# Kernel optimization log

Hardware: AMD Instinct MI355X
Metric: run time of the kernel (lower is better)

The kernel has to match this reference:

```python
import jax, jax.numpy as jnp
import numpy as np

B, D, STRIDE, OUT = 8192, 1024, 16, 64
L = D // STRIDE


def setup_inputs() -> dict:
    key = jax.random.key(0)
    kx, kw, kb = jax.random.split(key, 3)
    x = jax.random.normal(kx, (B, D), dtype=jnp.float32)
    # Stacked per-layer Dense kernels: layer i only sees features j < i*STRIDE.
    # Glorot-ish scale; masked entries are zeroed in reference() (faithful: they
    # don't exist in the original per-layer kernels).
    W = jax.random.normal(kw, (L, D, OUT), dtype=jnp.float32) * 0.02
    b = jax.random.normal(kb, (L, OUT), dtype=jnp.float32) * 0.02
    return {"x": x, "W": W, "b": b}


def reference(x, W, b):
    # Original: tf.stack([Dense_i(x[..., :i*stride]) for i in range(L)], -2)
    # Equivalent single causal-masked batched matmul.
    Lx, Dx, Ox = W.shape
    stride = Dx // Lx
    # mask[l, d] = 1 if feature d is visible to layer l (d < l*stride)
    mask = (jnp.arange(Dx)[None, :] < (jnp.arange(Lx) * stride)[:, None]).astype(W.dtype)
    Wm = W * mask[:, :, None]                      # [L, D, O]
    out = jnp.einsum("bd,ldo->blo", x, Wm) + b    # [B, L, O]
    return out
```

## Files before the change

kernel.cpp:

```cpp
#include <hip/hip_runtime.h>
#include <hip/hip_bf16.h>
#include <stdint.h>

#define BROWS 8192
#define DDIM  1024
#define LDIM  64
#define ODIM  64
#define NDIM  4096
#define KSTRIDE 16

typedef __attribute__((ext_vector_type(8))) short bf16x8;
typedef __attribute__((ext_vector_type(4))) float f32x4;
typedef __attribute__((ext_vector_type(8))) unsigned short u16x8;

static __device__ __forceinline__ unsigned short f2bf(float f) {
    union { float f; uint32_t u; } v; v.f = f;
    uint32_t r = 0x7FFFu + ((v.u >> 16) & 1u);
    return (unsigned short)((v.u + r) >> 16);
}

static __device__ __forceinline__ void async16(const void* g, void* l) {
    __builtin_amdgcn_global_load_lds(
        (const __attribute__((address_space(1))) void*)g,
        (__attribute__((address_space(3))) void*)l, 16, 0, 0);
}

__global__ __launch_bounds__(256) void cvt_x_kernel(const float* __restrict__ x,
                                                    unsigned short* __restrict__ xb) {
    int i = blockIdx.x * 256 + threadIdx.x;
    const float4* xf = reinterpret_cast<const float4*>(x);
    float4 v0 = xf[2 * i];
    float4 v1 = xf[2 * i + 1];
    u16x8 r;
    r[0] = f2bf(v0.x); r[1] = f2bf(v0.y); r[2] = f2bf(v0.z); r[3] = f2bf(v0.w);
    r[4] = f2bf(v1.x); r[5] = f2bf(v1.y); r[6] = f2bf(v1.z); r[7] = f2bf(v1.w);
    reinterpret_cast<u16x8*>(xb)[i] = r;
}

__global__ __launch_bounds__(256) void prep_w_kernel(const float* __restrict__ W,
                                                     unsigned short* __restrict__ wbt) {
    __shared__ float tile[64][65];
    const int l  = blockIdx.x >> 4;
    const int d0 = (blockIdx.x & 15) << 6;
    const int t  = threadIdx.x;
    {
        const int dd = t >> 2;
        const int o4 = (t & 3) << 4;
        const float* src = W + ((size_t)((l << 10) + d0 + dd) << 6) + o4;
        #pragma unroll
        for (int j = 0; j < 4; ++j) {
            float4 v = reinterpret_cast<const float4*>(src)[j];
            tile[dd][o4 + 4 * j + 0] = v.x;
            tile[dd][o4 + 4 * j + 1] = v.y;
            tile[dd][o4 + 4 * j + 2] = v.z;
            tile[dd][o4 + 4 * j + 3] = v.w;
        }
    }
    __syncthreads();
    {
        const int o    = t >> 2;
        const int dloc = (t & 3) << 4;
        const int kmax = l * KSTRIDE;
        unsigned short* dst = wbt + ((size_t)((l << 6) + o) << 10) + d0 + dloc;
        u16x8 r0, r1;
        #pragma unroll
        for (int j = 0; j < 8; ++j) {
            int da = d0 + dloc + j;
            int db = da + 8;
            r0[j] = (da < kmax) ? f2bf(tile[dloc + j][o])     : (unsigned short)0;
            r1[j] = (db < kmax) ? f2bf(tile[dloc + 8 + j][o]) : (unsigned short)0;
        }
        *reinterpret_cast<u16x8*>(dst)     = r0;
        *reinterpret_cast<u16x8*>(dst + 8) = r1;
    }
}

__global__ __launch_bounds__(256, 2) void ar_gemm_kernel(
        const unsigned short* __restrict__ xb,
        const unsigned short* __restrict__ wbt,
        const float* __restrict__ bias,
        float* __restrict__ out) {
    __shared__ unsigned short As[128 * 32];
    __shared__ unsigned short Bs[128 * 32];

    const int bm   = blockIdx.x & 63;
    const int bn   = 31 - (blockIdx.x >> 6);
    const int tid  = threadIdx.x;
    const int lane = tid & 63;
    const int wave = tid >> 6;
    const int wr   = wave >> 1;
    const int wc   = wave & 1;

    const int nkt = ((2 * bn + 1) * KSTRIDE + 31) >> 5;

    const int rc = lane >> 2;
    const int cb = (lane & 3) << 4;
    const char* gA0 = (const char*)xb  + ((size_t)(bm * 128 + (2 * wave + 0) * 16 + rc) * 2048) + cb;
    const char* gA1 = (const char*)xb  + ((size_t)(bm * 128 + (2 * wave + 1) * 16 + rc) * 2048) + cb;
    const char* gB0 = (const char*)wbt + ((size_t)(bn * 128 + (2 * wave + 0) * 16 + rc) * 2048) + cb;
    const char* gB1 = (const char*)wbt + ((size_t)(bn * 128 + (2 * wave + 1) * 16 + rc) * 2048) + cb;
    char* lA0 = (char*)As + (2 * wave + 0) * 1024;
    char* lA1 = (char*)As + (2 * wave + 1) * 1024;
    char* lB0 = (char*)Bs + (2 * wave + 0) * 1024;
    char* lB1 = (char*)Bs + (2 * wave + 1) * 1024;

    const int aoff = ((wr << 6) + (lane & 15)) * 64 + ((lane >> 4) << 4);
    const int boff = ((wc << 6) + (lane & 15)) * 64 + ((lane >> 4) << 4);

    f32x4 acc[4][4];
    #pragma unroll
    for (int m = 0; m < 4; ++m)
        #pragma unroll
        for (int n = 0; n < 4; ++n)
            acc[m][n] = (f32x4)(0.f);

    for (int kt = 0; kt < nkt; ++kt) {
        const int kb = kt << 6;
        async16(gA0 + kb, lA0);
        async16(gA1 + kb, lA1);
        async16(gB0 + kb, lB0);
        async16(gB1 + kb, lB1);
        __syncthreads();
        bf16x8 a[4], b[4];
        #pragma unroll
        for (int m = 0; m < 4; ++m)
            a[m] = *reinterpret_cast<const bf16x8*>((const char*)As + aoff + m * 1024);
        #pragma unroll
        for (int n = 0; n < 4; ++n)
            b[n] = *reinterpret_cast<const bf16x8*>((const char*)Bs + boff + n * 1024);
        #pragma unroll
        for (int m = 0; m < 4; ++m)
            #pragma unroll
            for (int n = 0; n < 4; ++n)
                acc[m][n] = __builtin_amdgcn_mfma_f32_16x16x32_bf16(a[m], b[n], acc[m][n], 0, 0, 0);
        __syncthreads();
    }

    const int crow = (bm << 7) + (wr << 6) + ((lane >> 4) << 2);
    const int ccol = (bn << 7) + (wc << 6) + (lane & 15);
    float bv[4];
    #pragma unroll
    for (int n = 0; n < 4; ++n) bv[n] = bias[ccol + n * 16];
    #pragma unroll
    for (int m = 0; m < 4; ++m)
        #pragma unroll
        for (int n = 0; n < 4; ++n)
            #pragma unroll
            for (int j = 0; j < 4; ++j)
                out[(size_t)(crow + m * 16 + j) * NDIM + ccol + n * 16] = acc[m][n][j] + bv[n];
}

__global__ __launch_bounds__(256) void naive_kernel(const float* __restrict__ x,
                                                    const float* __restrict__ W,
                                                    const float* __restrict__ bias,
                                                    float* __restrict__ out) {
    size_t idx = (size_t)blockIdx.x * 256 + threadIdx.x;
    if (idx >= (size_t)BROWS * NDIM) return;
    int m = (int)(idx >> 12);
    int n = (int)(idx & 4095);
    int l = n >> 6;
    int o = n & 63;
    int kmax = l * KSTRIDE;
    float s = bias[n];
    const float* xr = x + (size_t)m * DDIM;
    const float* wp = W + ((size_t)l << 16) + o;
    for (int d = 0; d < kmax; ++d) s += xr[d] * wp[(size_t)d << 6];
    out[idx] = s;
}

extern "C" void kernel_launch(void* const* d_in, const int* in_sizes, int n_in,
                              void* d_out, int out_size, void* d_ws, size_t ws_size,
                              hipStream_t stream) {
    const float* x = (const float*)d_in[0];
    const float* W = (const float*)d_in[1];
    const float* b = (const float*)d_in[2];
    float* out = (float*)d_out;

    const size_t need = ((size_t)BROWS * DDIM + (size_t)NDIM * DDIM) * sizeof(unsigned short);
    if (ws_size < need) {
        int total = BROWS * NDIM;
        naive_kernel<<<(total + 255) / 256, 256, 0, stream>>>(x, W, b, out);
        return;
    }
    unsigned short* xbuf = (unsigned short*)d_ws;
    unsigned short* wbt  = xbuf + (size_t)BROWS * DDIM;

    cvt_x_kernel<<<(BROWS * DDIM) / (256 * 8), 256, 0, stream>>>(x, xbuf);
    prep_w_kernel<<<LDIM * 16, 256, 0, stream>>>(W, wbt);
    ar_gemm_kernel<<<64 * 32, 256, 0, stream>>>(xbuf, wbt, b, out);
}
```

Baseline: 66.70 us.

## Rewrite GEMM as 256x256 double-buffered pipelined kernel and fuse prep kernels

```diff
diff --git a/kernel.cpp b/kernel.cpp
--- a/kernel.cpp
+++ b/kernel.cpp
@@ -25,129 +25,199 @@
         (__attribute__((address_space(3))) void*)l, 16, 0, 0);
 }
 
-__global__ __launch_bounds__(256) void cvt_x_kernel(const float* __restrict__ x,
-                                                    unsigned short* __restrict__ xb) {
-    int i = blockIdx.x * 256 + threadIdx.x;
-    const float4* xf = reinterpret_cast<const float4*>(x);
-    float4 v0 = xf[2 * i];
-    float4 v1 = xf[2 * i + 1];
-    u16x8 r;
-    r[0] = f2bf(v0.x); r[1] = f2bf(v0.y); r[2] = f2bf(v0.z); r[3] = f2bf(v0.w);
-    r[4] = f2bf(v1.x); r[5] = f2bf(v1.y); r[6] = f2bf(v1.z); r[7] = f2bf(v1.w);
-    reinterpret_cast<u16x8*>(xb)[i] = r;
-}
-
-__global__ __launch_bounds__(256) void prep_w_kernel(const float* __restrict__ W,
-                                                     unsigned short* __restrict__ wbt) {
-    __shared__ float tile[64][65];
-    const int l  = blockIdx.x >> 4;
-    const int d0 = (blockIdx.x & 15) << 6;
-    const int t  = threadIdx.x;
-    {
-        const int dd = t >> 2;
-        const int o4 = (t & 3) << 4;
-        const float* src = W + ((size_t)((l << 10) + d0 + dd) << 6) + o4;
-        #pragma unroll
-        for (int j = 0; j < 4; ++j) {
-            float4 v = reinterpret_cast<const float4*>(src)[j];
-            tile[dd][o4 + 4 * j + 0] = v.x;
-            tile[dd][o4 + 4 * j + 1] = v.y;
-            tile[dd][o4 + 4 * j + 2] = v.z;
-            tile[dd][o4 + 4 * j + 3] = v.w;
-        }
+__global__ __launch_bounds__(256) void prep_kernel(const float* __restrict__ x,
+                                                   const float* __restrict__ W,
+                                                   unsigned short* __restrict__ xb,
+                                                   unsigned short* __restrict__ wbt) {
+    const int bid = blockIdx.x;
+    if (bid < 1024) {
+        __shared__ float tile[64][65];
+        const int l  = bid >> 4;
+        const int d0 = (bid & 15) << 6;
+        const int t  = threadIdx.x;
+        {
+            const int dd = t >> 2;
+            const int o4 = (t & 3) << 4;
+            const float* src = W + ((size_t)((l << 10) + d0 + dd) << 6) + o4;
+            #pragma unroll
+            for (int j = 0; j < 4; ++j) {
+                float4 v = reinterpret_cast<const float4*>(src)[j];
+                tile[dd][o4 + 4 * j + 0] = v.x;
+                tile[dd][o4 + 4 * j + 1] = v.y;
+                tile[dd][o4 + 4 * j + 2] = v.z;
+                tile[dd][o4 + 4 * j + 3] = v.w;
+            }
+        }
+        __syncthreads();
+        {
+            const int o    = t >> 2;
+            const int dloc = (t & 3) << 4;
+            const int kmax = l * KSTRIDE;
+            unsigned short* dst = wbt + ((size_t)((l << 6) + o) << 10) + d0 + dloc;
+            u16x8 r0, r1;
+            #pragma unroll
+            for (int j = 0; j < 8; ++j) {
+                int da = d0 + dloc + j;
+                int db = da + 8;
+                r0[j] = (da < kmax) ? f2bf(tile[dloc + j][o])     : (unsigned short)0;
+                r1[j] = (db < kmax) ? f2bf(tile[dloc + 8 + j][o]) : (unsigned short)0;
+            }
+            *reinterpret_cast<u16x8*>(dst)     = r0;
+            *reinterpret_cast<u16x8*>(dst + 8) = r1;
+        }
+    } else {
+        int i = (bid - 1024) * 256 + threadIdx.x;
+        const float4* xf = reinterpret_cast<const float4*>(x);
+        float4 v0 = xf[2 * i];
+        float4 v1 = xf[2 * i + 1];
+        u16x8 r;
+        r[0] = f2bf(v0.x); r[1] = f2bf(v0.y); r[2] = f2bf(v0.z); r[3] = f2bf(v0.w);
+        r[4] = f2bf(v1.x); r[5] = f2bf(v1.y); r[6] = f2bf(v1.z); r[7] = f2bf(v1.w);
+        reinterpret_cast<u16x8*>(xb)[i] = r;
     }
-    __syncthreads();
-    {
-        const int o    = t >> 2;
-        const int dloc = (t & 3) << 4;
-        const int kmax = l * KSTRIDE;
-        unsigned short* dst = wbt + ((size_t)((l << 6) + o) << 10) + d0 + dloc;
-        u16x8 r0, r1;
-        #pragma unroll
-        for (int j = 0; j < 8; ++j) {
-            int da = d0 + dloc + j;
-            int db = da + 8;
-            r0[j] = (da < kmax) ? f2bf(tile[dloc + j][o])     : (unsigned short)0;
-            r1[j] = (db < kmax) ? f2bf(tile[dloc + 8 + j][o]) : (unsigned short)0;
-        }
-        *reinterpret_cast<u16x8*>(dst)     = r0;
-        *reinterpret_cast<u16x8*>(dst + 8) = r1;
-    }
-}
-
-__global__ __launch_bounds__(256, 2) void ar_gemm_kernel(
+}
+
+#define MMQ(I0, J0, B) \
+    _Pragma("unroll") \
+    for (int ii = 0; ii < 4; ++ii) \
+    _Pragma("unroll") \
+    for (int jj = 0; jj < 2; ++jj) \
+    _Pragma("unroll") \
+    for (int kk = 0; kk < 2; ++kk) \
+        acc[(I0) + ii][(J0) + jj] = __builtin_amdgcn_mfma_f32_16x16x32_bf16( \
+            a[ii][kk], B[jj][kk], acc[(I0) + ii][(J0) + jj], 0, 0, 0);
+
+#define BAR_MID() do { __builtin_amdgcn_s_barrier(); \
+    asm volatile("s_waitcnt lgkmcnt(0)" ::: "memory"); \
+    __builtin_amdgcn_sched_barrier(0); } while (0)
+#define BAR_END() do { __builtin_amdgcn_sched_barrier(0); \
+    __builtin_amdgcn_s_barrier(); } while (0)
+#define VMW4() asm volatile("s_waitcnt vmcnt(4)" ::: "memory")
+
+__global__ __launch_bounds__(512, 2) void ar_gemm_kernel(
         const unsigned short* __restrict__ xb,
         const unsigned short* __restrict__ wbt,
         const float* __restrict__ bias,
         float* __restrict__ out) {
-    __shared__ unsigned short As[128 * 32];
-    __shared__ unsigned short Bs[128 * 32];
-
-    const int bm   = blockIdx.x & 63;
-    const int bn   = 31 - (blockIdx.x >> 6);
+    __shared__ int4 smem[8192];
+    char* ldsc = (char*)smem;
+
     const int tid  = threadIdx.x;
     const int lane = tid & 63;
-    const int wave = tid >> 6;
-    const int wr   = wave >> 1;
-    const int wc   = wave & 1;
-
-    const int nkt = ((2 * bn + 1) * KSTRIDE + 31) >> 5;
-
-    const int rc = lane >> 2;
-    const int cb = (lane & 3) << 4;
-    const char* gA0 = (const char*)xb  + ((size_t)(bm * 128 + (2 * wave + 0) * 16 + rc) * 2048) + cb;
-    const char* gA1 = (const char*)xb  + ((size_t)(bm * 128 + (2 * wave + 1) * 16 + rc) * 2048) + cb;
-    const char* gB0 = (const char*)wbt + ((size_t)(bn * 128 + (2 * wave + 0) * 16 + rc) * 2048) + cb;
-    const char* gB1 = (const char*)wbt + ((size_t)(bn * 128 + (2 * wave + 1) * 16 + rc) * 2048) + cb;
-    char* lA0 = (char*)As + (2 * wave + 0) * 1024;
-    char* lA1 = (char*)As + (2 * wave + 1) * 1024;
-    char* lB0 = (char*)Bs + (2 * wave + 0) * 1024;
-    char* lB1 = (char*)Bs + (2 * wave + 1) * 1024;
-
-    const int aoff = ((wr << 6) + (lane & 15)) * 64 + ((lane >> 4) << 4);
-    const int boff = ((wc << 6) + (lane & 15)) * 64 + ((lane >> 4) << 4);
-
-    f32x4 acc[4][4];
+    const int wid  = tid >> 6;
+    const int wm   = wid >> 2;
+    const int wn   = wid & 3;
+    const int bid  = blockIdx.x;
+    const int bm   = bid & 31;
+    const int bn   = 15 - (bid >> 5);
+    const int nkt  = bn + 1;
+
+    const int gcol = (((tid & 7) ^ ((tid >> 3) & 7)) << 4);
+    const int srow = tid >> 3;
+
+    const int g0 = (((lane >> 4)     ^ (lane & 7)) << 4);
+    const int g1 = (((4 | (lane >> 4)) ^ (lane & 7)) << 4);
+    const int aoff = (wm * 128 + (lane & 15)) * 128;
+    const int boff = 32768 + (wn * 64 + (lane & 15)) * 128;
+
+    f32x4 acc[8][4];
     #pragma unroll
-    for (int m = 0; m < 4; ++m)
-        #pragma unroll
-        for (int n = 0; n < 4; ++n)
-            acc[m][n] = (f32x4)(0.f);
-
-    for (int kt = 0; kt < nkt; ++kt) {
-        const int kb = kt << 6;
-        async16(gA0 + kb, lA0);
-        async16(gA1 + kb, lA1);
-        async16(gB0 + kb, lB0);
-        async16(gB1 + kb, lB1);
-        __syncthreads();
-        bf16x8 a[4], b[4];
-        #pragma unroll
-        for (int m = 0; m < 4; ++m)
-            a[m] = *reinterpret_cast<const bf16x8*>((const char*)As + aoff + m * 1024);
-        #pragma unroll
-        for (int n = 0; n < 4; ++n)
-            b[n] = *reinterpret_cast<const bf16x8*>((const char*)Bs + boff + n * 1024);
-        #pragma unroll
-        for (int m = 0; m < 4; ++m)
-            #pragma unroll
-            for (int n = 0; n < 4; ++n)
-                acc[m][n] = __builtin_amdgcn_mfma_f32_16x16x32_bf16(a[m], b[n], acc[m][n], 0, 0, 0);
-        __syncthreads();
+    for (int i = 0; i < 8; ++i)
+        #pragma unroll
+        for (int j = 0; j < 4; ++j)
+            acc[i][j] = (f32x4)(0.f);
+
+    bf16x8 a[4][2], bL[2][2], bH[2][2];
+
+    auto stage = [&](int t, int part) {
+        const int ts = t < nkt ? t : nkt - 1;
+        char* l = ldsc + ((t & 1) << 16) + ((part >> 1) << 15) + ((part & 1) << 14) + tid * 16;
+        const unsigned short* srcm = (part >= 2) ? wbt : xb;
+        const int rb = (((part >= 2) ? bn : bm) << 8) + ((part & 1) << 7) + srow;
+        const char* g = (const char*)srcm + ((size_t)rb << 11) + ts * 128 + gcol;
+        async16(g, l);
+        async16(g + (64 << 11), l + 8192);
+    };
+    auto readA = [&](int par, int ih) {
+        const char* p = ldsc + (par << 16) + aoff + (ih << 13);
+        #pragma unroll
+        for (int ii = 0; ii < 4; ++ii) {
+            a[ii][0] = *(const bf16x8*)(p + ii * 2048 + g0);
+            a[ii][1] = *(const bf16x8*)(p + ii * 2048 + g1);
+        }
+    };
+    auto readB = [&](int par, int jh, bf16x8 (&b)[2][2]) {
+        const char* p = ldsc + (par << 16) + boff + (jh << 12);
+        #pragma unroll
+        for (int jj = 0; jj < 2; ++jj) {
+            b[jj][0] = *(const bf16x8*)(p + jj * 2048 + g0);
+            b[jj][1] = *(const bf16x8*)(p + jj * 2048 + g1);
+        }
+    };
+
+    stage(0, 0); stage(0, 1); stage(0, 2); stage(0, 3);
+    stage(1, 2); stage(1, 3);
+    VMW4();
+    __builtin_amdgcn_s_barrier();
+
+    const int niter = (nkt + 1) >> 1;
+    for (int J = 0; J < niter; ++J) {
+        const int T2 = 2 * J;
+        readA(0, 0); readB(0, 0, bL);
+        stage(T2 + 1, 0);
+        BAR_MID();
+        __builtin_amdgcn_s_setprio(1); MMQ(0, 0, bL); __builtin_amdgcn_s_setprio(0);
+        BAR_END();
+        readB(0, 1, bH);
+        stage(T2 + 1, 1);
+        BAR_MID();
+        __builtin_amdgcn_s_setprio(1); MMQ(0, 2, bH); __builtin_amdgcn_s_setprio(0);
+        BAR_END();
+        readA(0, 1);
+        stage(T2 + 2, 2);
+        BAR_MID();
+        __builtin_amdgcn_s_setprio(1); MMQ(4, 2, bH); __builtin_amdgcn_s_setprio(0);
+        BAR_END();
+        stage(T2 + 2, 3);
+        VMW4();
+        BAR_MID();
+        __builtin_amdgcn_s_setprio(1); MMQ(4, 0, bL); __builtin_amdgcn_s_setprio(0);
+        BAR_END();
+        if (T2 + 1 >= nkt) break;
+        readA(1, 0); readB(1, 0, bL);
+        stage(T2 + 2, 0);
+        BAR_MID();
+        __builtin_amdgcn_s_setprio(1); MMQ(0, 0, bL); __builtin_amdgcn_s_setprio(0);
+        BAR_END();
+        readB(1, 1, bH);
+        stage(T2 + 2, 1);
+        BAR_MID();
+        __builtin_amdgcn_s_setprio(1); MMQ(0, 2, bH); __builtin_amdgcn_s_setprio(0);
+        BAR_END();
+        readA(1, 1);
+        stage(T2 + 3, 2);
+        BAR_MID();
+        __builtin_amdgcn_s_setprio(1); MMQ(4, 2, bH); __builtin_amdgcn_s_setprio(0);
+        BAR_END();
+        stage(T2 + 3, 3);
+        VMW4();
+        BAR_MID();
+        __builtin_amdgcn_s_setprio(1); MMQ(4, 0, bL); __builtin_amdgcn_s_setprio(0);
+        BAR_END();
     }
 
-    const int crow = (bm << 7) + (wr << 6) + ((lane >> 4) << 2);
-    const int ccol = (bn << 7) + (wc << 6) + (lane & 15);
+    const int crow0 = (bm << 8) + (wm << 7) + ((lane >> 4) << 2);
+    const int ccol  = (bn << 8) + (wn << 6) + (lane & 15);
     float bv[4];
     #pragma unroll
-    for (int n = 0; n < 4; ++n) bv[n] = bias[ccol + n * 16];
+    for (int j = 0; j < 4; ++j) bv[j] = bias[ccol + j * 16];
     #pragma unroll
-    for (int m = 0; m < 4; ++m)
-        #pragma unroll
-        for (int n = 0; n < 4; ++n)
+    for (int i = 0; i < 8; ++i)
+        #pragma unroll
+        for (int j = 0; j < 4; ++j)
             #pragma unroll
-            for (int j = 0; j < 4; ++j)
-                out[(size_t)(crow + m * 16 + j) * NDIM + ccol + n * 16] = acc[m][n][j] + bv[n];
+            for (int q = 0; q < 4; ++q)
+                out[(size_t)(crow0 + i * 16 + q) * NDIM + ccol + j * 16] = acc[i][j][q] + bv[j];
 }
 
 __global__ __launch_bounds__(256) void naive_kernel(const float* __restrict__ x,
@@ -185,7 +255,6 @@
     unsigned short* xbuf = (unsigned short*)d_ws;
     unsigned short* wbt  = xbuf + (size_t)BROWS * DDIM;
 
-    cvt_x_kernel<<<(BROWS * DDIM) / (256 * 8), 256, 0, stream>>>(x, xbuf);
-    prep_w_kernel<<<LDIM * 16, 256, 0, stream>>>(W, wbt);
-    ar_gemm_kernel<<<64 * 32, 256, 0, stream>>>(xbuf, wbt, b, out);
-}
+    prep_kernel<<<5120, 256, 0, stream>>>(x, W, xbuf, wbt);
+    ar_gemm_kernel<<<512, 512, 0, stream>>>(xbuf, wbt, b, out);
+}
```

Measured after the change: 197.3 us. 2.96x slower.
